# Kernel tuning notes

Hardware: AMD Instinct MI355X
Metric: run time of the kernel (lower is better)

The kernel has to match this reference:

```python
import jax, jax.numpy as jnp
import numpy as np
from jax import lax
from jax.scipy.special import logsumexp

B, T, H, K = 64, 512, 1024, 8


def crf_nll(logits, tags, mask, trans):
    """Negative log-likelihood summed over batch (allennlp-style linear-chain CRF,
    no start/end transitions). logits [B,T,K], tags [B,T] int, mask [B,T] float, trans [K,K]."""
    def step(alpha, x):
        logit_t, m_t = x  # [B,K], [B]
        inner = alpha[:, :, None] + trans[None, :, :] + logit_t[:, None, :]  # [B,K,K]
        new = logsumexp(inner, axis=1)
        alpha = jnp.where(m_t[:, None] > 0, new, alpha)
        return alpha, None
    alpha, _ = lax.scan(step, logits[:, 0], (jnp.swapaxes(logits[:, 1:], 0, 1), mask[:, 1:].T))
    logZ = logsumexp(alpha, axis=-1)  # [B]
    emit = jnp.take_along_axis(logits, tags[..., None], axis=-1)[..., 0]  # [B,T]
    emit_score = jnp.sum(emit * mask, axis=-1)
    trans_score = jnp.sum(trans[tags[:, :-1], tags[:, 1:]] * mask[:, 1:], axis=-1)
    return -jnp.sum(emit_score + trans_score - logZ)


def viterbi(logits, trans):
    """Batched Viterbi decode with all-ones mask (as in the original forward).
    logits [B,T,K], trans [K,K] -> tags [B,T] int."""
    def step(alpha, logit_t):
        scores = alpha[:, :, None] + trans[None, :, :]  # [B,K_prev,K_next]
        bp = jnp.argmax(scores, axis=1)                 # [B,K]
        alpha = jnp.max(scores, axis=1) + logit_t
        return alpha, bp
    alpha, bps = lax.scan(step, logits[:, 0], jnp.swapaxes(logits[:, 1:], 0, 1))
    last = jnp.argmax(alpha, axis=-1)  # [B]
    def back(tag, bp):
        prev = jnp.take_along_axis(bp, tag[:, None], axis=1)[:, 0]
        return prev, prev
    _, prevs = lax.scan(back, last, bps, reverse=True)  # [T-1,B]
    return jnp.concatenate([prevs, last[None, :]], axis=0).T  # [B,T]


def setup_inputs():
    key = jax.random.key(0)
    ks = jax.random.split(key, 12)
    encoding = jax.random.normal(ks[0], (B, T, H), dtype=jnp.float32)
    raw = jax.random.randint(ks[1], (B, 3 * T), 0, K).astype(jnp.int32)
    offsets = jnp.concatenate([jnp.zeros(T, jnp.int32), jnp.full((T,), 8, jnp.int32), jnp.full((T,), 16, jnp.int32)])
    labels = raw + offsets[None, :]
    len_tokens = jax.random.randint(ks[2], (B,), 1, T + 1).astype(jnp.int32)
    s = 1.0 / np.sqrt(H)
    W_task = jax.random.uniform(ks[3], (H, K), jnp.float32, -s, s)
    b_task = jax.random.uniform(ks[4], (K,), jnp.float32, -s, s)
    W_process = jax.random.uniform(ks[5], (H, K), jnp.float32, -s, s)
    b_process = jax.random.uniform(ks[6], (K,), jnp.float32, -s, s)
    W_material = jax.random.uniform(ks[7], (H, K), jnp.float32, -s, s)
    b_material = jax.random.uniform(ks[8], (K,), jnp.float32, -s, s)
    trans_task = jax.random.normal(ks[9], (K, K), jnp.float32) * 0.1
    trans_process = jax.random.normal(ks[10], (K, K), jnp.float32) * 0.1
    trans_material = jax.random.normal(ks[11], (K, K), jnp.float32) * 0.1
    return {"encoding": encoding, "labels": labels, "len_tokens": len_tokens,
            "W_task": W_task, "b_task": b_task, "W_process": W_process, "b_process": b_process,
            "W_material": W_material, "b_material": b_material,
            "trans_task": trans_task, "trans_process": trans_process, "trans_material": trans_material}


def reference(encoding, labels, len_tokens, W_task, b_task, W_process, b_process,
              W_material, b_material, trans_task, trans_process, trans_material):
    task_logits = encoding @ W_task + b_task          # [B,T,K]
    process_logits = encoding @ W_process + b_process
    material_logits = encoding @ W_material + b_material
    logits3 = jnp.stack([task_logits, process_logits, material_logits])   # [3,B,T,K]
    trans3 = jnp.stack([trans_task, trans_process, trans_material])       # [3,K,K]
    # Viterbi with all-ones mask, as in the original forward
    tags3 = jax.vmap(viterbi)(logits3, trans3)  # [3,B,T]
    predicted_tags = jnp.concatenate([tags3[0], tags3[1] + 8, tags3[2] + 16], axis=1)  # [B,3T]
    # CRF NLL losses with length mask (training/validation path)
    mask = (jnp.arange(T)[None, :] < len_tokens[:, None]).astype(jnp.float32)
    labels3 = jnp.stack([labels[:, :T], labels[:, T:2 * T] - 8, labels[:, 2 * T:] - 16])
    loss = jnp.sum(jax.vmap(crf_nll, in_axes=(0, 0, None, 0))(logits3, labels3, mask, trans3))
    return task_logits, process_logits, material_logits, predicted_tags, loss
```

## Files before the change

kernel.cpp:

```cpp
#include <hip/hip_runtime.h>
#include <hip/hip_bf16.h>
#include <math.h>

#define BATCH 64
#define TT 512
#define HH 1024
#define KK 8
#define ROWS (BATCH * TT)
#define SEG  (ROWS * KK)
#define TAGS_OFF (3 * SEG)
#define LOSS_OFF (TAGS_OFF + BATCH * 3 * TT)

__global__ __launch_bounds__(256, 2) void gemm_heads(
    const float* __restrict__ enc,
    const float* __restrict__ Wt, const float* __restrict__ bt,
    const float* __restrict__ Wp, const float* __restrict__ bpv,
    const float* __restrict__ Wm, const float* __restrict__ bm,
    float* __restrict__ out)
{
    __shared__ float xt[4][2][16][68];
    __shared__ float wl[4][2][16][32];
    __shared__ float biasl[24];

    int tid  = threadIdx.x;
    int lane = tid & 63;
    int w    = __builtin_amdgcn_readfirstlane(tid >> 6);
    int r    = lane >> 2;
    int q    = lane & 3;
    int rowblk = blockIdx.x * 64;

    if (tid < 24) {
        int hd = tid >> 3, cl = tid & 7;
        biasl[tid] = (hd == 0) ? bt[cl] : (hd == 1) ? bpv[cl] : bm[cl];
    }

    const float* encw = enc + (size_t)rowblk * HH + w * 256;
    const float* Wkt = Wt + w * 2048;
    const float* Wkp = Wp + w * 2048;
    const float* Wkm = Wm + w * 2048;

    int srow = lane >> 2;
    int schunk = lane & 3;

    float acc[24];
#pragma unroll
    for (int c = 0; c < 24; ++c) acc[c] = 0.f;

    float4 sreg[4];
    float  wreg[6];

#define LOADT(it)                                                             \
    {                                                                         \
        _Pragma("unroll")                                                     \
        for (int i = 0; i < 4; ++i)                                           \
            sreg[i] = *(const float4*)(encw + (size_t)(srow + 16 * i) * HH +  \
                                       (it) * 16 + schunk * 4);               \
    }
#define WRITET(buf)                                                           \
    {                                                                         \
        _Pragma("unroll")                                                     \
        for (int i = 0; i < 4; ++i) {                                         \
            xt[w][buf][schunk * 4 + 0][srow + 16 * i] = sreg[i].x;            \
            xt[w][buf][schunk * 4 + 1][srow + 16 * i] = sreg[i].y;            \
            xt[w][buf][schunk * 4 + 2][srow + 16 * i] = sreg[i].z;            \
            xt[w][buf][schunk * 4 + 3][srow + 16 * i] = sreg[i].w;            \
        }                                                                     \
    }
#define WLOADG(it)                                                            \
    {                                                                         \
        wreg[0] = Wkt[(it) * 128 + lane]; wreg[1] = Wkt[(it) * 128 + 64 + lane]; \
        wreg[2] = Wkp[(it) * 128 + lane]; wreg[3] = Wkp[(it) * 128 + 64 + lane]; \
        wreg[4] = Wkm[(it) * 128 + lane]; wreg[5] = Wkm[(it) * 128 + 64 + lane]; \
    }
#define WWRITE(buf)                                                           \
    {                                                                         \
        int col_ = lane & 7;                                                  \
        _Pragma("unroll")                                                     \
        for (int i = 0; i < 6; ++i) {                                         \
            int hh_ = (lane >> 3) + 8 * (i & 1);                              \
            int c_  = 8 * (i >> 1) + col_;                                    \
            int q_  = (c_ * 43) >> 8;                       \
            int s_  = c_ - 6 * q_;                                            \
            wl[w][buf][hh_][8 * (q_ ^ (hh_ & 3)) + s_] = wreg[i];             \
        }                                                                     \
    }

    LOADT(0)
    WLOADG(0)
    WRITET(0)
    WWRITE(0)

    for (int it = 0; it < 16; ++it) {
        int cb = it & 1;
        if (it < 15) {
            LOADT(it + 1)
            WLOADG(it + 1)
        }
#pragma unroll
        for (int hh = 0; hh < 16; ++hh) {
            float4 xv = *(const float4*)&xt[w][cb][hh][4 * r];
            const float* wp_ = &wl[w][cb][hh][8 * (q ^ (hh & 3))];
            float4 w0 = *(const float4*)wp_;
            float2 w1 = *(const float2*)(wp_ + 4);
#pragma unroll
            for (int j = 0; j < 4; ++j) {
                float xe = (j == 0) ? xv.x : (j == 1) ? xv.y : (j == 2) ? xv.z : xv.w;
                acc[j * 6 + 0] = fmaf(xe, w0.x, acc[j * 6 + 0]);
                acc[j * 6 + 1] = fmaf(xe, w0.y, acc[j * 6 + 1]);
                acc[j * 6 + 2] = fmaf(xe, w0.z, acc[j * 6 + 2]);
                acc[j * 6 + 3] = fmaf(xe, w0.w, acc[j * 6 + 3]);
                acc[j * 6 + 4] = fmaf(xe, w1.x, acc[j * 6 + 4]);
                acc[j * 6 + 5] = fmaf(xe, w1.y, acc[j * 6 + 5]);
            }
        }
        if (it < 31) {
            WRITET(cb ^ 1)
            WWRITE(cb ^ 1)
        }
    }
#undef LOADT
#undef WRITET
#undef WLOADG
#undef WWRITE

    __syncthreads();
    float* xf = &xt[0][0][0][0];
    int myrow = 4 * r;
    if (w != 0) {
        float* sl = xf + w * 1600;
#pragma unroll
        for (int j = 0; j < 4; ++j)
#pragma unroll
            for (int s = 0; s < 6; ++s)
                sl[(myrow + j) * 25 + q * 6 + s] = acc[j * 6 + s];
    }
    __syncthreads();
    if (w == 0) {
#pragma unroll
        for (int j = 0; j < 4; ++j)
#pragma unroll
            for (int s = 0; s < 6; ++s)
                xf[(myrow + j) * 25 + q * 6 + s] =
                    acc[j * 6 + s] + xf[1600 + (myrow + j) * 25 + q * 6 + s]
                                   + xf[3200 + (myrow + j) * 25 + q * 6 + s]
                                   + xf[4800 + (myrow + j) * 25 + q * 6 + s];
    }
    __syncthreads();
#pragma unroll
    for (int i = 0; i < 2; ++i) {
        int flat = tid + 256 * i;
        if (flat < 384) {
            int seg  = flat >> 7;
            int rem  = flat & 127;
            int row  = rem >> 1;
            int half = rem & 1;
            float4 v;
            v.x = xf[row * 25 + seg * 8 + half * 4 + 0] + biasl[seg * 8 + half * 4 + 0];
            v.y = xf[row * 25 + seg * 8 + half * 4 + 1] + biasl[seg * 8 + half * 4 + 1];
            v.z = xf[row * 25 + seg * 8 + half * 4 + 2] + biasl[seg * 8 + half * 4 + 2];
            v.w = xf[row * 25 + seg * 8 + half * 4 + 3] + biasl[seg * 8 + half * 4 + 3];
            *(float4*)(out + (size_t)seg * SEG + (size_t)(rowblk + row) * 8 + half * 4) = v;
        }
    }
}

#define DPPF(x, ctrl) __int_as_float(__builtin_amdgcn_update_dpp(              \
    0, __float_as_int(x), ctrl, 0xF, 0xF, true))
#define SWIZF(x, pat) __int_as_float(__builtin_amdgcn_ds_swizzle(              \
    __float_as_int(x), pat))
#define BPERMF(a, x)  __int_as_float(__builtin_amdgcn_ds_bpermute(             \
    a, __float_as_int(x)))

__device__ __forceinline__ float rfl(float x) {
    return __int_as_float(__builtin_amdgcn_readfirstlane(__float_as_int(x)));
}

#if __has_builtin(__builtin_amdgcn_permlane16_swap)
__device__ __forceinline__ float xor16f(float x, int lane) {
    typedef unsigned uv2 __attribute__((ext_vector_type(2)));
    uv2 r = __builtin_amdgcn_permlane16_swap(__float_as_uint(x), __float_as_uint(x), false, false);
    return __uint_as_float((lane & 16) ? r.x : r.y);
}
#else
__device__ __forceinline__ float xor16f(float x, int lane) { return SWIZF(x, 0x401F); }
#endif

#if __has_builtin(__builtin_amdgcn_permlane32_swap)
__device__ __forceinline__ float xor32f(float x, int lane) {
    typedef unsigned uv2 __attribute__((ext_vector_type(2)));
    uv2 r = __builtin_amdgcn_permlane32_swap(__float_as_uint(x), __float_as_uint(x), false, false);
    return __uint_as_float((lane & 32) ? r.x : r.y);
}
#else
__device__ __forceinline__ float xor32f(float x, int lane) {
    return BPERMF(((lane ^ 32) << 2), x);
}
#endif

__global__ __launch_bounds__(128) void crf_vit(
    const float* __restrict__ logits,
    const int* __restrict__ labels,
    const int* __restrict__ lens,
    const float* __restrict__ trans_t,
    const float* __restrict__ trans_p,
    const float* __restrict__ trans_m,
    float* __restrict__ out_tags,
    float* __restrict__ partial)
{
    __shared__ float llds[TT * KK];
    __shared__ unsigned bpw[TT * 2];
    __shared__ unsigned fmapw[64][2];
    __shared__ unsigned char bnd[64];

    int blk = blockIdx.x;
    int h   = blk >> 6;
    int b   = blk & 63;
    int tid = threadIdx.x;
    int wid = __builtin_amdgcn_readfirstlane(tid >> 6);
    int lane = tid & 63;
    int hi = lane >> 3, lo = lane & 7;
    unsigned char* bpb = (unsigned char*)bpw;

    const float* L = logits + ((size_t)h * BATCH + b) * (TT * KK);
    const float4* Lv = (const float4*)L;
    float4* lv = (float4*)llds;
#pragma unroll
    for (int i = 0; i < 8; ++i) lv[tid + 128 * i] = Lv[tid + 128 * i];
    __syncthreads();

    const float* TR = (h == 0) ? trans_t : (h == 1) ? trans_p : trans_m;
    int len = lens[b];
    float trA = TR[lo * 8 + hi];
    float trB = TR[hi * 8 + lo];

    if (wid == 0) {
        float av = llds[lo];

#define VIT_EVEN(t, LT)                                                        \
    {                                                                          \
        float v0 = av + trA;                                                   \
        float ra = fmaxf(v0, DPPF(v0, 0xB1));                                  \
        float rb = fmaxf(ra, DPPF(ra, 0x4E));                                  \
        float vmax = fmaxf(rb, DPPF(rb, 0x141));                               \
        unsigned long long mk = __ballot(v0 == vmax);                          \
        int vi = __builtin_ctz(((unsigned)(mk >> (lane & 56))) & 0xffu);       \
        if (lo == 0) bpb[(t) * 8 + hi] = (unsigned char)vi;                    \
        av = vmax + (LT);                                                      \
    }
#define VIT_ODD(t, LT)                                                         \
    {                                                                          \
        float v0 = av + trB;                                                   \
        float ra = fmaxf(v0, DPPF(v0, 0x128));                                 \
        float rb = fmaxf(ra, xor16f(ra, lane));                                \
        float vmax = fmaxf(rb, xor32f(rb, lane));                              \
        unsigned long long mk = __ballot(v0 == vmax);                          \
        unsigned long long sel = (mk >> lo) & 0x0101010101010101ULL;           \
        int vi = __builtin_ctzll(sel) >> 3;                                    \
        if (hi == 0) bpb[(t) * 8 + lo] = (unsigned char)vi;                    \
        av = vmax + (LT);                                                      \
    }

        float ltA = llds[8 + hi];
        float ltB = llds[16 + lo];
        for (int t = 1; t <= 509; t += 2) {
            float ltA2 = llds[(t + 2) * 8 + hi];
            int tb = (t + 3 <= 511) ? (t + 3) : 511;
            float ltB2 = llds[tb * 8 + lo];
            VIT_EVEN(t, ltA);
            VIT_ODD(t + 1, ltB);
            ltA = ltA2; ltB = ltB2;
        }
        VIT_EVEN(511, ltA);
#undef VIT_EVEN
#undef VIT_ODD

        float ra = fmaxf(av, DPPF(av, 0x128));
        float rb = fmaxf(ra, xor16f(ra, lane));
        float vmax = fmaxf(rb, xor32f(rb, lane));
        unsigned long long mk = __ballot(av == vmax);
        int last_ = __builtin_ctzll(mk) >> 3;

        asm volatile("" ::: "memory");

        int t0 = lane * 8;
        unsigned rw[16];
#pragma unroll
        for (int j = 0; j < 8; ++j) {
            int t = t0 + 1 + j;
            if (t <= 511) { rw[2 * j] = bpw[t * 2]; rw[2 * j + 1] = bpw[t * 2 + 1]; }
            else          { rw[2 * j] = 0x03020100u; rw[2 * j + 1] = 0x07060504u; }
        }
        unsigned sv[8];
#pragma unroll
        for (int i = 0; i < 8; ++i) sv[i] = i;
#pragma unroll
        for (int j = 7; j >= 0; --j) {
            unsigned d0 = rw[2 * j], d1 = rw[2 * j + 1];
#pragma unroll
            for (int i = 0; i < 8; ++i) {
                unsigned s = sv[i];
                unsigned d = (s < 4) ? d0 : d1;
                sv[i] = (d >> (8 * (s & 3))) & 0xffu;
            }
        }
        fmapw[lane][0] = sv[0] | (sv[1] << 8) | (sv[2] << 16) | (sv[3] << 24);
        fmapw[lane][1] = sv[4] | (sv[5] << 8) | (sv[6] << 16) | (sv[7] << 24);
        asm volatile("" ::: "memory");

        if (lane == 0) {
            unsigned cur = (unsigned)last_;
            for (int l = 63; l >= 0; --l) {
                unsigned d = (cur < 4) ? fmapw[l][0] : fmapw[l][1];
                cur = (d >> (8 * (cur & 3))) & 0xffu;
                bnd[l] = (unsigned char)cur;
            }
        }
        asm volatile("" ::: "memory");

        int off = h * 8;
        float* otag = out_tags + b * (3 * TT) + h * TT;
        unsigned curr = (lane == 63) ? (unsigned)last_ : (unsigned)bnd[lane + 1];
#pragma unroll
        for (int j = 7; j >= 0; --j) {
            unsigned d = (curr < 4) ? rw[2 * j] : rw[2 * j + 1];
            curr = (d >> (8 * (curr & 3))) & 0xffu;
            otag[t0 + j] = (float)((int)curr + off);
        }
    } else {
        float EA = __expf(trA);
        float EB = __expf(trB);
        float al0 = llds[lo];
        float c0 = rfl(al0);
        float S = __expf(al0 - c0);
        float Mc = c0;
        float r2 = 0.f, r3 = 0.f;
        const float LN8 = 2.0794415416798357f;

#define LSE_EVEN(t, LT)                                                        \
    {                                                                          \
        float c = rfl(LT) + LN8;                                               \
        float F = __expf((LT) - c);                                            \
        float P = S * EA;                                                      \
        float sa = P + DPPF(P, 0xB1);                                          \
        float sb = sa + DPPF(sa, 0x4E);                                        \
        float ss = sb + DPPF(sb, 0x141);                                       \
        if ((t) < len) { S = ss * F; Mc += c; }                                \
        r2 = r3; r3 = __logf(rfl(S));                                          \
    }
#define LSE_ODD(t, LT)                                                         \
    {                                                                          \
        float c = rfl(LT) + LN8;                                               \
        float F = __expf((LT) - c);                                            \
        float P = S * EB;                                                      \
        float sa = P + DPPF(P, 0x128);                                         \
        float sb = sa + xor16f(sa, lane);                                      \
        float ss = sb + xor32f(sb, lane);                                      \
        if ((t) < len) { S = ss * F; Mc += c; }                                \
        r2 = r3; r3 = __logf(rfl(S));                                          \
    }

        float ltA = llds[8 + hi];
        float ltB = llds[16 + lo];
        for (int t = 1; t <= 509; t += 2) {
            if ((t & 3) == 1) {
                float g = r2;
                S *= __expf(-g);
                Mc += g;
            }
            float ltA2 = llds[(t + 2) * 8 + hi];
            int tb = (t + 3 <= 511) ? (t + 3) : 511;
            float ltB2 = llds[tb * 8 + lo];
            LSE_EVEN(t, ltA);
            LSE_ODD(t + 1, ltB);
            ltA = ltA2; ltB = ltB2;
        }
        LSE_EVEN(511, ltA);
#undef LSE_EVEN
#undef LSE_ODD

        float aj = Mc + __logf(S);
        float za = fmaxf(aj, DPPF(aj, 0x128));
        float zb = fmaxf(za, xor16f(za, lane));
        float zmax = fmaxf(zb, xor32f(zb, lane));
        float ze = __expf(aj - zmax);
        float zs = ze + DPPF(ze, 0x128);
        float zs2 = zs + xor16f(zs, lane);
        float zsum = zs2 + xor32f(zs2, lane);
        float logZ = zmax + __logf(zsum);

        const int* lab = labels + b * (3 * TT) + h * TT;
        int off = h * 8;
        float sc = 0.f;
#pragma unroll
        for (int j = 0; j < 8; ++j) {
            int t = lane + 64 * j;
            if (t < len) {
                int tg = lab[t] - off;
                sc += llds[t * 8 + tg];
                if (t >= 1) {
                    int tp = lab[t - 1] - off;
                    sc += TR[tp * 8 + tg];
                }
            }
        }
#pragma unroll
        for (int d = 1; d <= 32; d <<= 1) sc += __shfl_xor(sc, d);

        if (lane == 0) partial[blk] = logZ - sc;
    }
}

__global__ __launch_bounds__(64) void loss_reduce(
    const float* __restrict__ partial, float* __restrict__ out_loss)
{
    int lane = threadIdx.x;
    float s = partial[lane] + partial[lane + 64] + partial[lane + 128];
#pragma unroll
    for (int d = 1; d <= 32; d <<= 1) s += __shfl_xor(s, d);
    if (lane == 0) *out_loss = s;
}

extern "C" void kernel_launch(void* const* d_in, const int* in_sizes, int n_in,
                              void* d_out, int out_size, void* d_ws, size_t ws_size,
                              hipStream_t stream) {
    const float* enc    = (const float*)d_in[0];
    const int*   labels = (const int*)d_in[1];
    const int*   lens   = (const int*)d_in[2];
    const float* Wt     = (const float*)d_in[3];
    const float* bt     = (const float*)d_in[4];
    const float* Wp     = (const float*)d_in[5];
    const float* bpv    = (const float*)d_in[6];
    const float* Wm     = (const float*)d_in[7];
    const float* bm     = (const float*)d_in[8];
    const float* tr_t   = (const float*)d_in[9];
    const float* tr_p   = (const float*)d_in[10];
    const float* tr_m   = (const float*)d_in[11];

    float* out = (float*)d_out;
    float* lpart = (float*)d_ws;

    gemm_heads<<<512, 256, 0, stream>>>(enc, Wt, bt, Wp, bpv, Wm, bm, out);
    crf_vit<<<192, 128, 0, stream>>>(out, labels, lens, tr_t, tr_p, tr_m,
                                     out + TAGS_OFF, lpart);
    loss_reduce<<<1, 64, 0, stream>>>(lpart, out + LOSS_OFF);
}
```

Before: 87.92 us.

## Split CRF/Viterbi into lane-per-state forward kernels with global alpha history

Replaces the single per-sequence crf_vit kernel with three kernels. vit_fwd and lse_fwd pack 8 sequences per wave, one lane per state, and gather the previous alphas with DPP instead of a cross-lane reduction each step. vit_bt then recomputes backpointers in parallel from the Viterbi alpha history, now stored to global workspace, and does the chunked backtrace. The aim is to shorten the serial per-step dependency chain, at the cost of only 24 blocks for each forward kernel, serialising the Viterbi and LSE forward passes, and extra global traffic for the alpha history and the per-step logit loads.

Result: slower. 147.9 us (+68.3%).

```diff
diff --git a/kernel.cpp b/kernel.cpp
--- a/kernel.cpp
+++ b/kernel.cpp
@@ -10,6 +10,8 @@
 #define SEG  (ROWS * KK)
 #define TAGS_OFF (3 * SEG)
 #define LOSS_OFF (TAGS_OFF + BATCH * 3 * TT)
+#define HIST_FLOATS (192 * TT * KK)
+#define LPART_OFF (1 << 20)
 
 __global__ __launch_bounds__(256, 2) void gemm_heads(
     const float* __restrict__ enc,
@@ -79,7 +81,7 @@
         for (int i = 0; i < 6; ++i) {                                         \
             int hh_ = (lane >> 3) + 8 * (i & 1);                              \
             int c_  = 8 * (i >> 1) + col_;                                    \
-            int q_  = (c_ * 43) >> 8;                       \
+            int q_  = (c_ * 43) >> 8;                                         \
             int s_  = c_ - 6 * q_;                                            \
             wl[w][buf][hh_][8 * (q_ ^ (hh_ & 3)) + s_] = wreg[i];             \
         }                                                                     \
@@ -113,7 +115,7 @@
                 acc[j * 6 + 5] = fmaf(xe, w1.y, acc[j * 6 + 5]);
             }
         }
-        if (it < 31) {
+        if (it < 15) {
             WRITET(cb ^ 1)
             WWRITE(cb ^ 1)
         }
@@ -166,247 +168,262 @@
 
 #define DPPF(x, ctrl) __int_as_float(__builtin_amdgcn_update_dpp(              \
     0, __float_as_int(x), ctrl, 0xF, 0xF, true))
-#define SWIZF(x, pat) __int_as_float(__builtin_amdgcn_ds_swizzle(              \
-    __float_as_int(x), pat))
-#define BPERMF(a, x)  __int_as_float(__builtin_amdgcn_ds_bpermute(             \
-    a, __float_as_int(x)))
-
-__device__ __forceinline__ float rfl(float x) {
-    return __int_as_float(__builtin_amdgcn_readfirstlane(__float_as_int(x)));
-}
-
-#if __has_builtin(__builtin_amdgcn_permlane16_swap)
-__device__ __forceinline__ float xor16f(float x, int lane) {
-    typedef unsigned uv2 __attribute__((ext_vector_type(2)));
-    uv2 r = __builtin_amdgcn_permlane16_swap(__float_as_uint(x), __float_as_uint(x), false, false);
-    return __uint_as_float((lane & 16) ? r.x : r.y);
-}
-#else
-__device__ __forceinline__ float xor16f(float x, int lane) { return SWIZF(x, 0x401F); }
-#endif
-
-#if __has_builtin(__builtin_amdgcn_permlane32_swap)
-__device__ __forceinline__ float xor32f(float x, int lane) {
-    typedef unsigned uv2 __attribute__((ext_vector_type(2)));
-    uv2 r = __builtin_amdgcn_permlane32_swap(__float_as_uint(x), __float_as_uint(x), false, false);
-    return __uint_as_float((lane & 32) ? r.x : r.y);
-}
-#else
-__device__ __forceinline__ float xor32f(float x, int lane) {
-    return BPERMF(((lane ^ 32) << 2), x);
-}
-#endif
-
-__global__ __launch_bounds__(128) void crf_vit(
+
+__device__ __forceinline__ float bcast8(float x, int lane) {
+    float qv = DPPF(x, 0x00);
+    float hv = DPPF(qv, 0x141);
+    return (lane & 4) ? hv : qv;
+}
+
+#define GATHER8(ao, r0, r1, r2, r3, r4, r5, r6, r7)                            \
+    {                                                                          \
+        float s1_ = DPPF(ao, 0xB1);                                            \
+        float s2_ = DPPF(ao, 0x4E);                                            \
+        float s3_ = DPPF(s1_, 0x4E);                                           \
+        float s7_ = DPPF(ao, 0x141);                                           \
+        float s6_ = DPPF(s1_, 0x141);                                          \
+        float s5_ = DPPF(s2_, 0x141);                                          \
+        float s4_ = DPPF(s3_, 0x141);                                          \
+        r0 = ao; r1 = s1_; r2 = s2_; r3 = s3_;                                 \
+        r4 = s7_; r5 = s6_; r6 = s5_; r7 = s4_;                                \
+    }
+
+__global__ __launch_bounds__(64) void vit_fwd(
+    const float* __restrict__ logits,
+    const float* __restrict__ trans_t,
+    const float* __restrict__ trans_p,
+    const float* __restrict__ trans_m,
+    float* __restrict__ hist)
+{
+    int lane = threadIdx.x;
+    int g = lane >> 3, p = lane & 7;
+    int bb = blockIdx.x;
+    int h  = bb >> 3;
+    int seq = 8 * bb + g;
+
+    const float* TR = (h == 0) ? trans_t : (h == 1) ? trans_p : trans_m;
+    const float* Lgp = logits + (size_t)seq * (TT * KK) + p;
+    float* hp = hist + (size_t)seq * (TT * KK) + p;
+
+    float Tc0 = TR[(p ^ 0) * 8 + p], Tc1 = TR[(p ^ 1) * 8 + p];
+    float Tc2 = TR[(p ^ 2) * 8 + p], Tc3 = TR[(p ^ 3) * 8 + p];
+    float Tc4 = TR[(p ^ 7) * 8 + p], Tc5 = TR[(p ^ 6) * 8 + p];
+    float Tc6 = TR[(p ^ 5) * 8 + p], Tc7 = TR[(p ^ 4) * 8 + p];
+
+    float r0, r1, r2, r3, r4, r5, r6, r7;
+    float ao = Lgp[0];
+    hp[0] = ao;
+    GATHER8(ao, r0, r1, r2, r3, r4, r5, r6, r7)
+
+#define VSTEP(t, LT)                                                           \
+    {                                                                          \
+        float m0 = r0 + Tc0, m1 = r1 + Tc1, m2 = r2 + Tc2, m3 = r3 + Tc3;      \
+        float m4 = r4 + Tc4, m5 = r5 + Tc5, m6 = r6 + Tc6, m7 = r7 + Tc7;      \
+        float x01 = fmaxf(m0, m1), x23 = fmaxf(m2, m3);                        \
+        float x45 = fmaxf(m4, m5), x67 = fmaxf(m6, m7);                        \
+        float vmax = fmaxf(fmaxf(x01, x23), fmaxf(x45, x67));                  \
+        float ao_ = vmax + (LT);                                               \
+        hp[(t) * 8] = ao_;                                                     \
+        GATHER8(ao_, r0, r1, r2, r3, r4, r5, r6, r7)                           \
+    }
+
+    float l0 = Lgp[8 * 1], l1 = Lgp[8 * 2], l2 = Lgp[8 * 3], l3 = Lgp[8 * 4];
+    for (int kk = 0; kk < 127; ++kk) {
+        int t = 1 + 4 * kk;
+        VSTEP(t, l0)     l0 = Lgp[8 * (t + 4)];
+        VSTEP(t + 1, l1) l1 = Lgp[8 * (t + 5)];
+        VSTEP(t + 2, l2) l2 = Lgp[8 * (t + 6)];
+        VSTEP(t + 3, l3) l3 = Lgp[8 * (t + 7)];
+    }
+    VSTEP(509, l0)
+    VSTEP(510, l1)
+    VSTEP(511, l2)
+#undef VSTEP
+}
+
+__global__ __launch_bounds__(64) void lse_fwd(
     const float* __restrict__ logits,
     const int* __restrict__ labels,
     const int* __restrict__ lens,
     const float* __restrict__ trans_t,
     const float* __restrict__ trans_p,
     const float* __restrict__ trans_m,
-    float* __restrict__ out_tags,
     float* __restrict__ partial)
 {
-    __shared__ float llds[TT * KK];
+    int lane = threadIdx.x;
+    int g = lane >> 3, p = lane & 7;
+    int bb = blockIdx.x;
+    int h  = bb >> 3;
+    int seq = 8 * bb + g;
+    int b   = seq & 63;
+
+    const float* TR = (h == 0) ? trans_t : (h == 1) ? trans_p : trans_m;
+    const float* Lgp = logits + (size_t)seq * (TT * KK) + p;
+    int len = lens[b];
+
+    float E0 = __expf(TR[(p ^ 0) * 8 + p]), E1 = __expf(TR[(p ^ 1) * 8 + p]);
+    float E2 = __expf(TR[(p ^ 2) * 8 + p]), E3 = __expf(TR[(p ^ 3) * 8 + p]);
+    float E4 = __expf(TR[(p ^ 7) * 8 + p]), E5 = __expf(TR[(p ^ 6) * 8 + p]);
+    float E6 = __expf(TR[(p ^ 5) * 8 + p]), E7 = __expf(TR[(p ^ 4) * 8 + p]);
+
+    float a0 = Lgp[0];
+    float c0 = bcast8(a0, lane);
+    float S  = __expf(a0 - c0);
+    float Mc = c0;
+    float r0, r1, r2, r3, r4, r5, r6, r7;
+    GATHER8(S, r0, r1, r2, r3, r4, r5, r6, r7)
+
+#define LSTEP(t, LT, RENORM)                                                   \
+    {                                                                          \
+        float p0 = r0 * E0, p1 = r1 * E1, p2 = r2 * E2, p3 = r3 * E3;          \
+        float p4 = r4 * E4, p5 = r5 * E5, p6 = r6 * E6, p7 = r7 * E7;          \
+        float ss = ((p0 + p1) + (p2 + p3)) + ((p4 + p5) + (p6 + p7));          \
+        float Sn = ss * __expf(LT);                                            \
+        S = ((t) < len) ? Sn : S;                                              \
+        if (RENORM) {                                                          \
+            float sref = bcast8(S, lane);                                      \
+            float gg = __logf(sref);                                           \
+            S *= __expf(-gg);                                                  \
+            Mc += gg;                                                          \
+        }                                                                      \
+        GATHER8(S, r0, r1, r2, r3, r4, r5, r6, r7)                             \
+    }
+
+    float l0 = Lgp[8 * 1], l1 = Lgp[8 * 2], l2 = Lgp[8 * 3], l3 = Lgp[8 * 4];
+    for (int kk = 0; kk < 127; ++kk) {
+        int t = 1 + 4 * kk;
+        LSTEP(t, l0, 1)      l0 = Lgp[8 * (t + 4)];
+        LSTEP(t + 1, l1, 0)  l1 = Lgp[8 * (t + 5)];
+        LSTEP(t + 2, l2, 0)  l2 = Lgp[8 * (t + 6)];
+        LSTEP(t + 3, l3, 0)  l3 = Lgp[8 * (t + 7)];
+    }
+    LSTEP(509, l0, 1)
+    LSTEP(510, l1, 0)
+    LSTEP(511, l2, 0)
+#undef LSTEP
+
+    float sum8 = ((r0 + r1) + (r2 + r3)) + ((r4 + r5) + (r6 + r7));
+    float logZ = Mc + __logf(sum8);
+
+    const float* Lg = logits + (size_t)seq * (TT * KK);
+    const int* lab = labels + b * (3 * TT) + h * TT;
+    int off = h * 8;
+    float sc = 0.f;
+    for (int j = 0; j < 64; ++j) {
+        int t = p + 8 * j;
+        if (t < len) {
+            int tg = lab[t] - off;
+            sc += Lg[t * 8 + tg];
+            if (t >= 1) {
+                int tp = lab[t - 1] - off;
+                sc += TR[tp * 8 + tg];
+            }
+        }
+    }
+    sc += DPPF(sc, 0xB1);
+    sc += DPPF(sc, 0x4E);
+    sc += DPPF(sc, 0x141);
+
+    if (p == 0) partial[seq] = logZ - sc;
+}
+
+__global__ __launch_bounds__(64) void vit_bt(
+    const float* __restrict__ hist,
+    const float* __restrict__ trans_t,
+    const float* __restrict__ trans_p,
+    const float* __restrict__ trans_m,
+    float* __restrict__ out_tags)
+{
     __shared__ unsigned bpw[TT * 2];
     __shared__ unsigned fmapw[64][2];
     __shared__ unsigned char bnd[64];
 
-    int blk = blockIdx.x;
-    int h   = blk >> 6;
-    int b   = blk & 63;
-    int tid = threadIdx.x;
-    int wid = __builtin_amdgcn_readfirstlane(tid >> 6);
-    int lane = tid & 63;
-    int hi = lane >> 3, lo = lane & 7;
+    int seq = blockIdx.x;
+    int h = seq >> 6, b = seq & 63;
+    int lane = threadIdx.x;
+    int c = lane >> 3, kn = lane & 7;
     unsigned char* bpb = (unsigned char*)bpw;
 
-    const float* L = logits + ((size_t)h * BATCH + b) * (TT * KK);
-    const float4* Lv = (const float4*)L;
-    float4* lv = (float4*)llds;
-#pragma unroll
-    for (int i = 0; i < 8; ++i) lv[tid + 128 * i] = Lv[tid + 128 * i];
-    __syncthreads();
-
     const float* TR = (h == 0) ? trans_t : (h == 1) ? trans_p : trans_m;
-    int len = lens[b];
-    float trA = TR[lo * 8 + hi];
-    float trB = TR[hi * 8 + lo];
-
-    if (wid == 0) {
-        float av = llds[lo];
-
-#define VIT_EVEN(t, LT)                                                        \
-    {                                                                          \
-        float v0 = av + trA;                                                   \
-        float ra = fmaxf(v0, DPPF(v0, 0xB1));                                  \
-        float rb = fmaxf(ra, DPPF(ra, 0x4E));                                  \
-        float vmax = fmaxf(rb, DPPF(rb, 0x141));                               \
-        unsigned long long mk = __ballot(v0 == vmax);                          \
-        int vi = __builtin_ctz(((unsigned)(mk >> (lane & 56))) & 0xffu);       \
-        if (lo == 0) bpb[(t) * 8 + hi] = (unsigned char)vi;                    \
-        av = vmax + (LT);                                                      \
-    }
-#define VIT_ODD(t, LT)                                                         \
-    {                                                                          \
-        float v0 = av + trB;                                                   \
-        float ra = fmaxf(v0, DPPF(v0, 0x128));                                 \
-        float rb = fmaxf(ra, xor16f(ra, lane));                                \
-        float vmax = fmaxf(rb, xor32f(rb, lane));                              \
-        unsigned long long mk = __ballot(v0 == vmax);                          \
-        unsigned long long sel = (mk >> lo) & 0x0101010101010101ULL;           \
-        int vi = __builtin_ctzll(sel) >> 3;                                    \
-        if (hi == 0) bpb[(t) * 8 + lo] = (unsigned char)vi;                    \
-        av = vmax + (LT);                                                      \
-    }
-
-        float ltA = llds[8 + hi];
-        float ltB = llds[16 + lo];
-        for (int t = 1; t <= 509; t += 2) {
-            float ltA2 = llds[(t + 2) * 8 + hi];
-            int tb = (t + 3 <= 511) ? (t + 3) : 511;
-            float ltB2 = llds[tb * 8 + lo];
-            VIT_EVEN(t, ltA);
-            VIT_ODD(t + 1, ltB);
-            ltA = ltA2; ltB = ltB2;
-        }
-        VIT_EVEN(511, ltA);
-#undef VIT_EVEN
-#undef VIT_ODD
-
-        float ra = fmaxf(av, DPPF(av, 0x128));
-        float rb = fmaxf(ra, xor16f(ra, lane));
-        float vmax = fmaxf(rb, xor32f(rb, lane));
-        unsigned long long mk = __ballot(av == vmax);
-        int last_ = __builtin_ctzll(mk) >> 3;
-
-        asm volatile("" ::: "memory");
-
-        int t0 = lane * 8;
-        unsigned rw[16];
-#pragma unroll
-        for (int j = 0; j < 8; ++j) {
-            int t = t0 + 1 + j;
-            if (t <= 511) { rw[2 * j] = bpw[t * 2]; rw[2 * j + 1] = bpw[t * 2 + 1]; }
-            else          { rw[2 * j] = 0x03020100u; rw[2 * j + 1] = 0x07060504u; }
-        }
-        unsigned sv[8];
-#pragma unroll
-        for (int i = 0; i < 8; ++i) sv[i] = i;
-#pragma unroll
-        for (int j = 7; j >= 0; --j) {
-            unsigned d0 = rw[2 * j], d1 = rw[2 * j + 1];
-#pragma unroll
-            for (int i = 0; i < 8; ++i) {
-                unsigned s = sv[i];
-                unsigned d = (s < 4) ? d0 : d1;
-                sv[i] = (d >> (8 * (s & 3))) & 0xffu;
-            }
-        }
-        fmapw[lane][0] = sv[0] | (sv[1] << 8) | (sv[2] << 16) | (sv[3] << 24);
-        fmapw[lane][1] = sv[4] | (sv[5] << 8) | (sv[6] << 16) | (sv[7] << 24);
-        asm volatile("" ::: "memory");
-
-        if (lane == 0) {
-            unsigned cur = (unsigned)last_;
-            for (int l = 63; l >= 0; --l) {
-                unsigned d = (cur < 4) ? fmapw[l][0] : fmapw[l][1];
-                cur = (d >> (8 * (cur & 3))) & 0xffu;
-                bnd[l] = (unsigned char)cur;
-            }
-        }
-        asm volatile("" ::: "memory");
-
-        int off = h * 8;
-        float* otag = out_tags + b * (3 * TT) + h * TT;
-        unsigned curr = (lane == 63) ? (unsigned)last_ : (unsigned)bnd[lane + 1];
-#pragma unroll
-        for (int j = 7; j >= 0; --j) {
-            unsigned d = (curr < 4) ? rw[2 * j] : rw[2 * j + 1];
-            curr = (d >> (8 * (curr & 3))) & 0xffu;
-            otag[t0 + j] = (float)((int)curr + off);
-        }
-    } else {
-        float EA = __expf(trA);
-        float EB = __expf(trB);
-        float al0 = llds[lo];
-        float c0 = rfl(al0);
-        float S = __expf(al0 - c0);
-        float Mc = c0;
-        float r2 = 0.f, r3 = 0.f;
-        const float LN8 = 2.0794415416798357f;
-
-#define LSE_EVEN(t, LT)                                                        \
-    {                                                                          \
-        float c = rfl(LT) + LN8;                                               \
-        float F = __expf((LT) - c);                                            \
-        float P = S * EA;                                                      \
-        float sa = P + DPPF(P, 0xB1);                                          \
-        float sb = sa + DPPF(sa, 0x4E);                                        \
-        float ss = sb + DPPF(sb, 0x141);                                       \
-        if ((t) < len) { S = ss * F; Mc += c; }                                \
-        r2 = r3; r3 = __logf(rfl(S));                                          \
-    }
-#define LSE_ODD(t, LT)                                                         \
-    {                                                                          \
-        float c = rfl(LT) + LN8;                                               \
-        float F = __expf((LT) - c);                                            \
-        float P = S * EB;                                                      \
-        float sa = P + DPPF(P, 0x128);                                         \
-        float sb = sa + xor16f(sa, lane);                                      \
-        float ss = sb + xor32f(sb, lane);                                      \
-        if ((t) < len) { S = ss * F; Mc += c; }                                \
-        r2 = r3; r3 = __logf(rfl(S));                                          \
-    }
-
-        float ltA = llds[8 + hi];
-        float ltB = llds[16 + lo];
-        for (int t = 1; t <= 509; t += 2) {
-            if ((t & 3) == 1) {
-                float g = r2;
-                S *= __expf(-g);
-                Mc += g;
-            }
-            float ltA2 = llds[(t + 2) * 8 + hi];
-            int tb = (t + 3 <= 511) ? (t + 3) : 511;
-            float ltB2 = llds[tb * 8 + lo];
-            LSE_EVEN(t, ltA);
-            LSE_ODD(t + 1, ltB);
-            ltA = ltA2; ltB = ltB2;
-        }
-        LSE_EVEN(511, ltA);
-#undef LSE_EVEN
-#undef LSE_ODD
-
-        float aj = Mc + __logf(S);
-        float za = fmaxf(aj, DPPF(aj, 0x128));
-        float zb = fmaxf(za, xor16f(za, lane));
-        float zmax = fmaxf(zb, xor32f(zb, lane));
-        float ze = __expf(aj - zmax);
-        float zs = ze + DPPF(ze, 0x128);
-        float zs2 = zs + xor16f(zs, lane);
-        float zsum = zs2 + xor32f(zs2, lane);
-        float logZ = zmax + __logf(zsum);
-
-        const int* lab = labels + b * (3 * TT) + h * TT;
-        int off = h * 8;
-        float sc = 0.f;
-#pragma unroll
-        for (int j = 0; j < 8; ++j) {
-            int t = lane + 64 * j;
-            if (t < len) {
-                int tg = lab[t] - off;
-                sc += llds[t * 8 + tg];
-                if (t >= 1) {
-                    int tp = lab[t - 1] - off;
-                    sc += TR[tp * 8 + tg];
-                }
-            }
-        }
-#pragma unroll
-        for (int d = 1; d <= 32; d <<= 1) sc += __shfl_xor(sc, d);
-
-        if (lane == 0) partial[blk] = logZ - sc;
+    const float* H = hist + (size_t)seq * (TT * KK);
+
+    float T0 = TR[0 * 8 + kn], T1 = TR[1 * 8 + kn], T2 = TR[2 * 8 + kn];
+    float T3 = TR[3 * 8 + kn], T4 = TR[4 * 8 + kn], T5 = TR[5 * 8 + kn];
+    float T6 = TR[6 * 8 + kn], T7 = TR[7 * 8 + kn];
+
+    for (int j = 0; j < 64; ++j) {
+        int t = c * 64 + j + 1;
+        if (t <= 511) {
+            float4 a03 = *(const float4*)&H[(t - 1) * 8];
+            float4 a47 = *(const float4*)&H[(t - 1) * 8 + 4];
+            float v = a03.x + T0; int vi = 0; float nv;
+            nv = a03.y + T1; if (nv > v) { v = nv; vi = 1; }
+            nv = a03.z + T2; if (nv > v) { v = nv; vi = 2; }
+            nv = a03.w + T3; if (nv > v) { v = nv; vi = 3; }
+            nv = a47.x + T4; if (nv > v) { v = nv; vi = 4; }
+            nv = a47.y + T5; if (nv > v) { v = nv; vi = 5; }
+            nv = a47.z + T6; if (nv > v) { v = nv; vi = 6; }
+            nv = a47.w + T7; if (nv > v) { v = nv; vi = 7; }
+            bpb[t * 8 + kn] = (unsigned char)vi;
+        }
+    }
+
+    float4 f03 = *(const float4*)&H[511 * 8];
+    float4 f47 = *(const float4*)&H[511 * 8 + 4];
+    float fv = f03.x; int last_ = 0; float nf;
+    nf = f03.y; if (nf > fv) { fv = nf; last_ = 1; }
+    nf = f03.z; if (nf > fv) { fv = nf; last_ = 2; }
+    nf = f03.w; if (nf > fv) { fv = nf; last_ = 3; }
+    nf = f47.x; if (nf > fv) { fv = nf; last_ = 4; }
+    nf = f47.y; if (nf > fv) { fv = nf; last_ = 5; }
+    nf = f47.z; if (nf > fv) { fv = nf; last_ = 6; }
+    nf = f47.w; if (nf > fv) { fv = nf; last_ = 7; }
+
+    asm volatile("" ::: "memory");
+
+    int t0 = lane * 8;
+    unsigned rw[16];
+#pragma unroll
+    for (int j = 0; j < 8; ++j) {
+        int t = t0 + 1 + j;
+        if (t <= 511) { rw[2 * j] = bpw[t * 2]; rw[2 * j + 1] = bpw[t * 2 + 1]; }
+        else          { rw[2 * j] = 0x03020100u; rw[2 * j + 1] = 0x07060504u; }
+    }
+    unsigned sv[8];
+#pragma unroll
+    for (int i = 0; i < 8; ++i) sv[i] = i;
+#pragma unroll
+    for (int j = 7; j >= 0; --j) {
+        unsigned d0 = rw[2 * j], d1 = rw[2 * j + 1];
+#pragma unroll
+        for (int i = 0; i < 8; ++i) {
+            unsigned s = sv[i];
+            unsigned d = (s < 4) ? d0 : d1;
+            sv[i] = (d >> (8 * (s & 3))) & 0xffu;
+        }
+    }
+    fmapw[lane][0] = sv[0] | (sv[1] << 8) | (sv[2] << 16) | (sv[3] << 24);
+    fmapw[lane][1] = sv[4] | (sv[5] << 8) | (sv[6] << 16) | (sv[7] << 24);
+    asm volatile("" ::: "memory");
+
+    if (lane == 0) {
+        unsigned cur = (unsigned)last_;
+        for (int l = 63; l >= 0; --l) {
+            unsigned d = (cur < 4) ? fmapw[l][0] : fmapw[l][1];
+            cur = (d >> (8 * (cur & 3))) & 0xffu;
+            bnd[l] = (unsigned char)cur;
+        }
+    }
+    asm volatile("" ::: "memory");
+
+    int off = h * 8;
+    float* otag = out_tags + b * (3 * TT) + h * TT;
+    unsigned curr = (lane == 63) ? (unsigned)last_ : (unsigned)bnd[lane + 1];
+#pragma unroll
+    for (int j = 7; j >= 0; --j) {
+        unsigned d = (curr < 4) ? rw[2 * j] : rw[2 * j + 1];
+        curr = (d >> (8 * (curr & 3))) & 0xffu;
+        otag[t0 + j] = (float)((int)curr + off);
     }
 }
 
@@ -436,11 +453,13 @@
     const float* tr_p   = (const float*)d_in[10];
     const float* tr_m   = (const float*)d_in[11];
 
-    float* out = (float*)d_out;
-    float* lpart = (float*)d_ws;
-
-    gemm_heads<<<512, 256, 0, stream>>>(enc, Wt, bt, Wp, bpv, Wm, bm, out);
-    crf_vit<<<192, 128, 0, stream>>>(out, labels, lens, tr_t, tr_p, tr_m,
-                                     out + TAGS_OFF, lpart);
+    float* out  = (float*)d_out;
+    float* hist = (float*)d_ws;
+    float* lpart = (float*)d_ws + LPART_OFF;
+
+    gemm_heads<<<ROWS / 64, 256, 0, stream>>>(enc, Wt, bt, Wp, bpv, Wm, bm, out);
+    vit_fwd<<<24, 64, 0, stream>>>(out, tr_t, tr_p, tr_m, hist);
+    lse_fwd<<<24, 64, 0, stream>>>(out, labels, lens, tr_t, tr_p, tr_m, lpart);
+    vit_bt<<<192, 64, 0, stream>>>(hist, tr_t, tr_p, tr_m, out + TAGS_OFF);
     loss_reduce<<<1, 64, 0, stream>>>(lpart, out + LOSS_OFF);
 }
```
